# Performance work log

Hardware: AMD Instinct MI355X
Metric: run time of the kernel (lower is better)

The kernel has to match this reference:

```python
import jax, jax.numpy as jnp
import numpy as np

T2 = 0.05
EPS = 1e-05
N = 8192
D = 512
C = 16
COUNT = N // C


def setup_inputs() -> dict:
    key = jax.random.key(0)
    k1, k2 = jax.random.split(key)
    text = jax.random.normal(k1, (N, D), dtype=jnp.float32)
    image = jax.random.normal(k2, (N, D), dtype=jnp.float32)
    # label must contain exactly class_counts[i] samples of class i
    label = (jnp.arange(N) // COUNT).astype(jnp.int32)
    class_counts = jnp.full((C,), COUNT, dtype=jnp.int32)
    return {"text": text, "image": image, "label": label, "class_counts": class_counts}


def _normalize(x):
    # torch F.normalize(x, dim=1): x / max(||x||, 1e-12)
    n = jnp.sqrt(jnp.sum(x * x, axis=1, keepdims=True))
    return x / jnp.maximum(n, 1e-12)


def reference(text, image, label, class_counts):
    num_classes = class_counts.shape[0]
    onehot = jax.nn.one_hot(label, num_classes, dtype=text.dtype)  # [N, C]
    inv_count = 1.0 / class_counts.astype(text.dtype)              # [C]

    def loss_one(f):
        f = _normalize(f)
        # cosine similarity of unit vectors == dot product
        E = jnp.exp((f @ f.T) / T2)                 # [N, N]
        cls_sums = E @ onehot                       # [N, C]: per-row sum grouped by column class
        own = jnp.take_along_axis(cls_sums, label[:, None].astype(jnp.int32), axis=1)[:, 0]
        within = own - jnp.diagonal(E)              # mask out self-similarity (eye mask)
        other = (jnp.sum(cls_sums, axis=1) - own) / (num_classes - 1)
        # NOTE: original torch code aliases denominator_i = nominator_i and then
        # updates in place (+=), so nominator == denominator after the class loop.
        den = within + other
        per_row = -jnp.log(den / (den + EPS))
        return jnp.sum(per_row * inv_count[label])

    return loss_one(text) + loss_one(image)
```

## Files before the change

### kernel.cpp

```cpp
#include <hip/hip_runtime.h>
#include <stdint.h>

#define NROWS 8192
#define DDIM 512
#define NCLS 16
#define T2INV 20.0f
#define EPSV 1e-5f
#define NTILE 32
#define NOFF (NTILE * (NTILE - 1) / 2)
#define NBLK 1024

typedef int int32x4 __attribute__((ext_vector_type(4)));

__device__ __forceinline__ void async16(void* lds, const void* g) {
  auto gp = (__attribute__((address_space(1))) uint32_t*)(uintptr_t)g;
  auto lp = (__attribute__((address_space(3))) uint32_t*)(uintptr_t)lds;
  __builtin_amdgcn_global_load_lds(gp, lp, 16, 0, 0);
}

__device__ __forceinline__ uint32_t q8(float f) {
  float c = fmaxf(-127.f, fminf(127.f, f * 127.f));
  return (uint32_t)((int)rintf(c) & 255);
}

__global__ __launch_bounds__(256) void norm_kernel(const float* __restrict__ text,
                                                   const float* __restrict__ image,
                                                   uint8_t* __restrict__ out,
                                                   float* __restrict__ den,
                                                   float* __restrict__ out0) {
  const int w = threadIdx.x >> 6, l = threadIdx.x & 63;
  const int rid = blockIdx.x * 4 + w;
  const int m = rid >> 13;
  const int row = rid & (NROWS - 1);
  const float* src = (m ? image : text) + (size_t)row * DDIM;
  float4 v0 = ((const float4*)src)[l];
  float4 v1 = ((const float4*)src)[64 + l];
  float s = v0.x * v0.x + v0.y * v0.y + v0.z * v0.z + v0.w * v0.w +
            v1.x * v1.x + v1.y * v1.y + v1.z * v1.z + v1.w * v1.w;
  #pragma unroll
  for (int off = 32; off; off >>= 1) s += __shfl_xor(s, off);
  const float inv = 1.0f / fmaxf(sqrtf(s), 1e-12f);
  uint2 o;
  o.x = q8(v0.x * inv) | (q8(v0.y * inv) << 8) | (q8(v0.z * inv) << 16) |
        (q8(v0.w * inv) << 24);
  o.y = q8(v1.x * inv) | (q8(v1.y * inv) << 8) | (q8(v1.z * inv) << 16) |
        (q8(v1.w * inv) << 24);
  ((uint2*)(out + (size_t)rid * DDIM))[l] = o;
  if (l == 0) den[rid] = 0.0f;
  if (rid == 0 && l == 0) out0[0] = 0.0f;
}

__global__ __launch_bounds__(512, 2) void gram_kernel(const uint8_t* __restrict__ Fall,
                                                      float* __restrict__ denAll) {
  const int bid = blockIdx.x;
  const int bs = (bid & 7) * (NBLK / 8) + (bid >> 3);

  const int w = threadIdx.x >> 6, l = threadIdx.x & 63;
  const int wr = w >> 2, wc = w & 3;

  __shared__ __align__(16) uint8_t Ab[2][32768];
  __shared__ __align__(16) uint8_t Bb[2][32768];

  const int sbase = w * 8 + (l >> 3);
  const int skb = (((l & 7) ^ ((4 * w + (l >> 4)) & 7))) * 16;
  const size_t g0 = (size_t)sbase * DDIM + skb;

  uint32_t aoff[8], boff[4];
  #pragma unroll
  for (int f = 0; f < 8; ++f) {
    const int rowl = wr * 128 + f * 16 + (l & 15);
    aoff[f] = (uint32_t)(rowl * 128 + (((l >> 4) ^ ((rowl >> 1) & 7)) << 4));
  }
  #pragma unroll
  for (int f = 0; f < 4; ++f) {
    const int rowl = wc * 64 + f * 16 + (l & 15);
    boff[f] = (uint32_t)(rowl * 128 + (((l >> 4) ^ ((rowl >> 1) & 7)) << 4));
  }

  auto run_tile = [&](const uint8_t* __restrict__ F, float* __restrict__ den,
                      int q, int p, bool diag) {
    const bool dead = diag && (wr == 1) && (wc < 2);
    const uint8_t* sA = F + (size_t)q * 256 * DDIM + g0;
    const uint8_t* sB = F + (size_t)p * 256 * DDIM + g0;
    const uint8_t* bb0 = diag ? &Ab[0][0] : &Bb[0][0];

    int32x4 acc[8][4] = {};

    #define STAGE(buf, k0)                                                    \
      {                                                                       \
        _Pragma("unroll")                                                     \
        for (int i = 0; i < 4; ++i) {                                         \
          async16(&Ab[buf][w * 1024 + i * 8192], sA + i * 32768 + (k0));      \
          if (!diag)                                                          \
            async16(&Bb[buf][w * 1024 + i * 8192], sB + i * 32768 + (k0));    \
        }                                                                     \
      }

    STAGE(0, 0);
    #pragma unroll
    for (int ts = 0; ts < 4; ++ts) {
      asm volatile("s_waitcnt vmcnt(0)" ::: "memory");
      __builtin_amdgcn_s_barrier();
      if (ts < 3) STAGE((ts + 1) & 1, (ts + 1) * 128);
      if (!dead) {
        #pragma unroll
        for (int sub = 0; sub < 2; ++sub) {
          int32x4 b[4];
          #pragma unroll
          for (int f = 0; f < 4; ++f)
            b[f] = *(const int32x4*)(bb0 + (ts & 1) * 32768 +
                                     (boff[f] ^ (sub * 64)));
          #pragma unroll
          for (int fh = 0; fh < 2; ++fh) {
            int32x4 a[4];
            #pragma unroll
            for (int f = 0; f < 4; ++f)
              a[f] = *(const int32x4*)(&Ab[0][0] + (ts & 1) * 32768 +
                                       (aoff[fh * 4 + f] ^ (sub * 64)));
            __builtin_amdgcn_s_setprio(1);
            #pragma unroll
            for (int i = 0; i < 4; ++i) {
              #pragma unroll
              for (int j = 0; j < 4; ++j)
                acc[fh * 4 + i][j] = __builtin_amdgcn_mfma_i32_16x16x64_i8(
                    a[i], b[j], acc[fh * 4 + i][j], 0, 0, 0);
            }
            __builtin_amdgcn_s_setprio(0);
          }
        }
      }
    }
    #undef STAGE

    if (!dead) {
      const float SC = T2INV / 16129.0f;
      const float wgt = ((q >> 1) == (p >> 1)) ? 1.0f : (1.0f / 15.0f);
      const int rbase = q * 256 + wr * 128;
      const int cbase = p * 256 + wc * 64;
      float cs[4] = {0.f, 0.f, 0.f, 0.f};
      #pragma unroll
      for (int fi = 0; fi < 8; ++fi) {
        const int rg0 = rbase + fi * 16 + ((l >> 4) << 2);
        float rs[4] = {0.f, 0.f, 0.f, 0.f};
        #pragma unroll
        for (int fj = 0; fj < 4; ++fj) {
          const int cg = cbase + fj * 16 + (l & 15);
          #pragma unroll
          for (int r = 0; r < 4; ++r) {
            float e = __expf((float)acc[fi][fj][r] * SC);
            if (diag && rg0 + r >= cg) e = 0.0f;
            rs[r] += e;
            cs[fj] += e;
          }
        }
        #pragma unroll
        for (int r = 0; r < 4; ++r) {
          rs[r] += __shfl_xor(rs[r], 1);
          rs[r] += __shfl_xor(rs[r], 2);
          rs[r] += __shfl_xor(rs[r], 4);
          rs[r] += __shfl_xor(rs[r], 8);
        }
        if ((l & 15) == 0) {
          #pragma unroll
          for (int r = 0; r < 4; ++r) atomicAdd(&den[rg0 + r], wgt * rs[r]);
        }
      }
      #pragma unroll
      for (int fj = 0; fj < 4; ++fj) {
        cs[fj] += __shfl_xor(cs[fj], 16);
        cs[fj] += __shfl_xor(cs[fj], 32);
      }
      if (l < 16) {
        #pragma unroll
        for (int fj = 0; fj < 4; ++fj)
          atomicAdd(&den[cbase + fj * 16 + l], wgt * cs[fj]);
      }
    }
  };

  if (bs < 2 * NOFF) {
    const int mat = bs >= NOFF;
    const int t = bs - NOFF * mat;
    int p = (int)((1.0f + sqrtf(1.0f + 8.0f * (float)t)) * 0.5f);
    while ((p + 1) * p / 2 <= t) ++p;
    while (p * (p - 1) / 2 > t) --p;
    const int q = t - p * (p - 1) / 2;
    run_tile(Fall + (size_t)mat * NROWS * DDIM, denAll + (size_t)mat * NROWS,
             q, p, false);
  } else {
    const int d = bs - 2 * NOFF;
    const int mat = d >> 4, k = d & 15;
    const uint8_t* F = Fall + (size_t)mat * NROWS * DDIM;
    float* den = denAll + (size_t)mat * NROWS;
    run_tile(F, den, 2 * k, 2 * k, true);
    __syncthreads();
    run_tile(F, den, 2 * k + 1, 2 * k + 1, true);
  }
}

__global__ __launch_bounds__(256) void finalize_kernel(const float* __restrict__ den,
                                                       const int* __restrict__ label,
                                                       const int* __restrict__ counts,
                                                       float* __restrict__ out) {
  const int i = blockIdx.x * 256 + threadIdx.x;
  const float d = den[i];
  const float ic = 1.0f / (float)counts[label[i & (NROWS - 1)]];
  float s = log1pf(EPSV / d) * ic;
  #pragma unroll
  for (int off = 32; off; off >>= 1) s += __shfl_xor(s, off);
  if ((threadIdx.x & 63) == 0) atomicAdd(out, s);
}

__global__ void sentinel_kernel(float* out) { out[0] = -42.0f; }

extern "C" void kernel_launch(void* const* d_in, const int* in_sizes, int n_in,
                              void* d_out, int out_size, void* d_ws, size_t ws_size,
                              hipStream_t stream) {
  (void)in_sizes; (void)n_in; (void)out_size;
  const float* text  = (const float*)d_in[0];
  const float* image = (const float*)d_in[1];
  const int* label   = (const int*)d_in[2];
  const int* counts  = (const int*)d_in[3];

  const size_t fn_bytes = (size_t)2 * NROWS * DDIM;
  const size_t need = fn_bytes + (size_t)2 * NROWS * sizeof(float);
  if (ws_size < need) {
    sentinel_kernel<<<1, 1, 0, stream>>>((float*)d_out);
    return;
  }

  uint8_t* Fn = (uint8_t*)d_ws;
  float* den = (float*)((char*)d_ws + fn_bytes);

  norm_kernel<<<dim3((2 * NROWS) / 4), 256, 0, stream>>>(text, image, Fn, den,
                                                         (float*)d_out);
  gram_kernel<<<dim3(NBLK), 512, 0, stream>>>(Fn, den);
  finalize_kernel<<<dim3((2 * NROWS) / 256), 256, 0, stream>>>(den, label, counts,
                                                               (float*)d_out);
}
```

Baseline: 79.14 us.

## Process multiple tiles per block with cross-tile prefetch of the next tile

Halves the grid so each block processes two off-diagonal tiles (or four diagonal tiles), and remaps the tile assignment to fit. The first K-slice of the next tile is staged into LDS during the last K-step of the current tile, so its load overlaps compute and the epilogue. This cuts block launch overhead and hides the pipeline fill of each later tile. The cost is longer blocks, fewer blocks for load balancing, and more complex tile decoding.

```diff
diff --git a/kernel.cpp b/kernel.cpp
--- a/kernel.cpp
+++ b/kernel.cpp
@@ -7,8 +7,7 @@
 #define T2INV 20.0f
 #define EPSV 1e-5f
 #define NTILE 32
-#define NOFF (NTILE * (NTILE - 1) / 2)
-#define NBLK 1024
+#define NBLK 512
 
 typedef int int32x4 __attribute__((ext_vector_type(4)));
 
@@ -54,6 +53,8 @@
                                                       float* __restrict__ denAll) {
   const int bid = blockIdx.x;
   const int bs = (bid & 7) * (NBLK / 8) + (bid >> 3);
+  const bool diagQ = bs >= 496;
+  const int nt = diagQ ? 4 : 2;
 
   const int w = threadIdx.x >> 6, l = threadIdx.x & 63;
   const int wr = w >> 2, wc = w & 3;
@@ -77,31 +78,64 @@
     boff[f] = (uint32_t)(rowl * 128 + (((l >> 4) ^ ((rowl >> 1) & 7)) << 4));
   }
 
-  auto run_tile = [&](const uint8_t* __restrict__ F, float* __restrict__ den,
-                      int q, int p, bool diag) {
-    const bool dead = diag && (wr == 1) && (wc < 2);
-    const uint8_t* sA = F + (size_t)q * 256 * DDIM + g0;
-    const uint8_t* sB = F + (size_t)p * 256 * DDIM + g0;
-    const uint8_t* bb0 = diag ? &Ab[0][0] : &Bb[0][0];
+  auto decode = [&](int tl, int& mat, int& q, int& p) {
+    if (bs < 480) {
+      mat = bs >= 240;
+      const int u = bs - 240 * mat;
+      int qq = 0, acc = 0;
+      while (acc + ((31 - qq) >> 1) <= u) { acc += (31 - qq) >> 1; ++qq; }
+      q = qq;
+      p = qq + 1 + 2 * (u - acc) + tl;
+    } else if (bs < 496) {
+      const int i = bs - 480;
+      mat = i >= 8;
+      q = 4 * (i - 8 * mat) + 2 * tl;
+      p = 31;
+    } else {
+      const int d = bs - 496;
+      mat = d >= 8;
+      q = p = 4 * (d - 8 * mat) + tl;
+    }
+  };
+
+  auto stage = [&](const uint8_t* sA, const uint8_t* sB, bool diag, int buf,
+                   int k0) {
+    #pragma unroll
+    for (int i = 0; i < 4; ++i) {
+      async16(&Ab[buf][w * 1024 + i * 8192], sA + i * 32768 + k0);
+      if (!diag) async16(&Bb[buf][w * 1024 + i * 8192], sB + i * 32768 + k0);
+    }
+  };
+
+  int mc, qc, pc, mn, qn, pn;
+  decode(0, mc, qc, pc);
+  const uint8_t* Fc = Fall + (size_t)mc * NROWS * DDIM;
+  const uint8_t* sAc = Fc + (size_t)qc * 256 * DDIM + g0;
+  const uint8_t* sBc = Fc + (size_t)pc * 256 * DDIM + g0;
+  stage(sAc, sBc, diagQ, 0, 0);
+
+  for (int tl = 0; tl < nt; ++tl) {
+    const bool dead = diagQ && (wr == 1) && (wc < 2);
+    const uint8_t* bb0 = diagQ ? &Ab[0][0] : &Bb[0][0];
+    const bool havenext = (tl + 1 < nt);
+    const uint8_t *sAn = nullptr, *sBn = nullptr;
+    if (havenext) {
+      decode(tl + 1, mn, qn, pn);
+      const uint8_t* Fn_ = Fall + (size_t)mn * NROWS * DDIM;
+      sAn = Fn_ + (size_t)qn * 256 * DDIM + g0;
+      sBn = Fn_ + (size_t)pn * 256 * DDIM + g0;
+    }
 
     int32x4 acc[8][4] = {};
 
-    #define STAGE(buf, k0)                                                    \
-      {                                                                       \
-        _Pragma("unroll")                                                     \
-        for (int i = 0; i < 4; ++i) {                                         \
-          async16(&Ab[buf][w * 1024 + i * 8192], sA + i * 32768 + (k0));      \
-          if (!diag)                                                          \
-            async16(&Bb[buf][w * 1024 + i * 8192], sB + i * 32768 + (k0));    \
-        }                                                                     \
-      }
-
-    STAGE(0, 0);
     #pragma unroll
     for (int ts = 0; ts < 4; ++ts) {
       asm volatile("s_waitcnt vmcnt(0)" ::: "memory");
       __builtin_amdgcn_s_barrier();
-      if (ts < 3) STAGE((ts + 1) & 1, (ts + 1) * 128);
+      if (ts < 3)
+        stage(sAc, sBc, diagQ, (ts + 1) & 1, (ts + 1) * 128);
+      else if (havenext)
+        stage(sAn, sBn, diagQ, 0, 0);
       if (!dead) {
         #pragma unroll
         for (int sub = 0; sub < 2; ++sub) {
@@ -130,13 +164,13 @@
         }
       }
     }
-    #undef STAGE
 
     if (!dead) {
+      float* den = denAll + (size_t)mc * NROWS;
       const float SC = T2INV / 16129.0f;
-      const float wgt = ((q >> 1) == (p >> 1)) ? 1.0f : (1.0f / 15.0f);
-      const int rbase = q * 256 + wr * 128;
-      const int cbase = p * 256 + wc * 64;
+      const float wgt = ((qc >> 1) == (pc >> 1)) ? 1.0f : (1.0f / 15.0f);
+      const int rbase = qc * 256 + wr * 128;
+      const int cbase = pc * 256 + wc * 64;
       float cs[4] = {0.f, 0.f, 0.f, 0.f};
       #pragma unroll
       for (int fi = 0; fi < 8; ++fi) {
@@ -148,7 +182,7 @@
           #pragma unroll
           for (int r = 0; r < 4; ++r) {
             float e = __expf((float)acc[fi][fj][r] * SC);
-            if (diag && rg0 + r >= cg) e = 0.0f;
+            if (diagQ && rg0 + r >= cg) e = 0.0f;
             rs[r] += e;
             cs[fj] += e;
           }
@@ -176,25 +210,9 @@
           atomicAdd(&den[cbase + fj * 16 + l], wgt * cs[fj]);
       }
     }
-  };
-
-  if (bs < 2 * NOFF) {
-    const int mat = bs >= NOFF;
-    const int t = bs - NOFF * mat;
-    int p = (int)((1.0f + sqrtf(1.0f + 8.0f * (float)t)) * 0.5f);
-    while ((p + 1) * p / 2 <= t) ++p;
-    while (p * (p - 1) / 2 > t) --p;
-    const int q = t - p * (p - 1) / 2;
-    run_tile(Fall + (size_t)mat * NROWS * DDIM, denAll + (size_t)mat * NROWS,
-             q, p, false);
-  } else {
-    const int d = bs - 2 * NOFF;
-    const int mat = d >> 4, k = d & 15;
-    const uint8_t* F = Fall + (size_t)mat * NROWS * DDIM;
-    float* den = denAll + (size_t)mat * NROWS;
-    run_tile(F, den, 2 * k, 2 * k, true);
-    __syncthreads();
-    run_tile(F, den, 2 * k + 1, 2 * k + 1, true);
+
+    mc = mn; qc = qn; pc = pn;
+    if (havenext) { sAc = sAn; sBc = sBn; }
   }
 }
 
```

Result: slower. 101.0 us (+27.7%).

## Retile int8 Gram kernel to 128x128 tiles with 256-thread blocks

Applied to the files above, without the earlier changes.

The Gram tile shrinks from 256x256 to 128x128, and the tile grid grows to 64x64 upper-triangle tiles across 4096 blocks. Each block now uses 4 waves with a 2x2 warp layout, a 64-byte K-slab per stage over 8 stages, and a reworked LDS swizzle. The goal is more concurrent blocks per CU and better load balance across the many CUs. The cost is more global and LDS traffic per MFMA and twice as many atomic row and column reductions.

```diff
diff --git a/kernel.cpp b/kernel.cpp
--- a/kernel.cpp
+++ b/kernel.cpp
@@ -6,9 +6,9 @@
 #define NCLS 16
 #define T2INV 20.0f
 #define EPSV 1e-5f
-#define NTILE 32
+#define NTILE 64
 #define NOFF (NTILE * (NTILE - 1) / 2)
-#define NBLK 1024
+#define NBLK 4096
 
 typedef int int32x4 __attribute__((ext_vector_type(4)));
 
@@ -50,96 +50,84 @@
   if (rid == 0 && l == 0) out0[0] = 0.0f;
 }
 
-__global__ __launch_bounds__(512, 2) void gram_kernel(const uint8_t* __restrict__ Fall,
+__global__ __launch_bounds__(256, 4) void gram_kernel(const uint8_t* __restrict__ Fall,
                                                       float* __restrict__ denAll) {
   const int bid = blockIdx.x;
   const int bs = (bid & 7) * (NBLK / 8) + (bid >> 3);
 
   const int w = threadIdx.x >> 6, l = threadIdx.x & 63;
-  const int wr = w >> 2, wc = w & 3;
-
-  __shared__ __align__(16) uint8_t Ab[2][32768];
-  __shared__ __align__(16) uint8_t Bb[2][32768];
-
-  const int sbase = w * 8 + (l >> 3);
-  const int skb = (((l & 7) ^ ((4 * w + (l >> 4)) & 7))) * 16;
-  const size_t g0 = (size_t)sbase * DDIM + skb;
-
-  uint32_t aoff[8], boff[4];
-  #pragma unroll
-  for (int f = 0; f < 8; ++f) {
-    const int rowl = wr * 128 + f * 16 + (l & 15);
-    aoff[f] = (uint32_t)(rowl * 128 + (((l >> 4) ^ ((rowl >> 1) & 7)) << 4));
-  }
+  const int wr = w >> 1, wc = w & 1;
+
+  __shared__ __align__(16) uint8_t Ab[2][8192];
+  __shared__ __align__(16) uint8_t Bb[2][8192];
+
+  const int srow = w * 16 + (l >> 2);
+  const int skb = ((l & 3) ^ ((l >> 3) & 3)) * 16;
+  const size_t g0 = (size_t)srow * DDIM + skb;
+
+  uint32_t aoff[4], boff[4];
   #pragma unroll
   for (int f = 0; f < 4; ++f) {
-    const int rowl = wc * 64 + f * 16 + (l & 15);
-    boff[f] = (uint32_t)(rowl * 128 + (((l >> 4) ^ ((rowl >> 1) & 7)) << 4));
+    const int ra = wr * 64 + f * 16 + (l & 15);
+    aoff[f] = (uint32_t)(ra * 64 + ((((l >> 4) ^ ((ra >> 1) & 3))) << 4));
+    const int rb = wc * 64 + f * 16 + (l & 15);
+    boff[f] = (uint32_t)(rb * 64 + ((((l >> 4) ^ ((rb >> 1) & 3))) << 4));
   }
 
   auto run_tile = [&](const uint8_t* __restrict__ F, float* __restrict__ den,
                       int q, int p, bool diag) {
-    const bool dead = diag && (wr == 1) && (wc < 2);
-    const uint8_t* sA = F + (size_t)q * 256 * DDIM + g0;
-    const uint8_t* sB = F + (size_t)p * 256 * DDIM + g0;
+    const bool dead = diag && (wr == 1) && (wc == 0);
+    const uint8_t* sA = F + (size_t)q * 128 * DDIM + g0;
+    const uint8_t* sB = F + (size_t)p * 128 * DDIM + g0;
     const uint8_t* bb0 = diag ? &Ab[0][0] : &Bb[0][0];
 
-    int32x4 acc[8][4] = {};
+    int32x4 acc[4][4] = {};
 
     #define STAGE(buf, k0)                                                    \
       {                                                                       \
         _Pragma("unroll")                                                     \
-        for (int i = 0; i < 4; ++i) {                                         \
-          async16(&Ab[buf][w * 1024 + i * 8192], sA + i * 32768 + (k0));      \
+        for (int i = 0; i < 2; ++i) {                                         \
+          async16(&Ab[buf][w * 1024 + i * 4096], sA + i * 32768 + (k0));      \
           if (!diag)                                                          \
-            async16(&Bb[buf][w * 1024 + i * 8192], sB + i * 32768 + (k0));    \
+            async16(&Bb[buf][w * 1024 + i * 4096], sB + i * 32768 + (k0));    \
         }                                                                     \
       }
 
     STAGE(0, 0);
     #pragma unroll
-    for (int ts = 0; ts < 4; ++ts) {
+    for (int ts = 0; ts < 8; ++ts) {
       asm volatile("s_waitcnt vmcnt(0)" ::: "memory");
       __builtin_amdgcn_s_barrier();
-      if (ts < 3) STAGE((ts + 1) & 1, (ts + 1) * 128);
+      if (ts < 7) STAGE((ts + 1) & 1, (ts + 1) * 64);
       if (!dead) {
-        #pragma unroll
-        for (int sub = 0; sub < 2; ++sub) {
-          int32x4 b[4];
+        int32x4 a[4], b[4];
+        #pragma unroll
+        for (int f = 0; f < 4; ++f)
+          b[f] = *(const int32x4*)(bb0 + (ts & 1) * 8192 + boff[f]);
+        #pragma unroll
+        for (int f = 0; f < 4; ++f)
+          a[f] = *(const int32x4*)(&Ab[0][0] + (ts & 1) * 8192 + aoff[f]);
+        __builtin_amdgcn_s_setprio(1);
+        #pragma unroll
+        for (int i = 0; i < 4; ++i) {
           #pragma unroll
-          for (int f = 0; f < 4; ++f)
-            b[f] = *(const int32x4*)(bb0 + (ts & 1) * 32768 +
-                                     (boff[f] ^ (sub * 64)));
-          #pragma unroll
-          for (int fh = 0; fh < 2; ++fh) {
-            int32x4 a[4];
-            #pragma unroll
-            for (int f = 0; f < 4; ++f)
-              a[f] = *(const int32x4*)(&Ab[0][0] + (ts & 1) * 32768 +
-                                       (aoff[fh * 4 + f] ^ (sub * 64)));
-            __builtin_amdgcn_s_setprio(1);
-            #pragma unroll
-            for (int i = 0; i < 4; ++i) {
-              #pragma unroll
-              for (int j = 0; j < 4; ++j)
-                acc[fh * 4 + i][j] = __builtin_amdgcn_mfma_i32_16x16x64_i8(
-                    a[i], b[j], acc[fh * 4 + i][j], 0, 0, 0);
-            }
-            __builtin_amdgcn_s_setprio(0);
-          }
-        }
+          for (int j = 0; j < 4; ++j)
+            acc[i][j] = __builtin_amdgcn_mfma_i32_16x16x64_i8(
+                a[i], b[j], acc[i][j], 0, 0, 0);
+        }
+        __builtin_amdgcn_s_setprio(0);
       }
     }
     #undef STAGE
 
     if (!dead) {
       const float SC = T2INV / 16129.0f;
-      const float wgt = ((q >> 1) == (p >> 1)) ? 1.0f : (1.0f / 15.0f);
-      const int rbase = q * 256 + wr * 128;
-      const int cbase = p * 256 + wc * 64;
+      const float wgt = ((q >> 2) == (p >> 2)) ? 1.0f : (1.0f / 15.0f);
+      const int rbase = q * 128 + wr * 64;
+      const int cbase = p * 128 + wc * 64;
       float cs[4] = {0.f, 0.f, 0.f, 0.f};
       #pragma unroll
-      for (int fi = 0; fi < 8; ++fi) {
+      for (int fi = 0; fi < 4; ++fi) {
         const int rg0 = rbase + fi * 16 + ((l >> 4) << 2);
         float rs[4] = {0.f, 0.f, 0.f, 0.f};
         #pragma unroll
@@ -189,7 +177,7 @@
              q, p, false);
   } else {
     const int d = bs - 2 * NOFF;
-    const int mat = d >> 4, k = d & 15;
+    const int mat = d >> 5, k = d & 31;
     const uint8_t* F = Fall + (size_t)mat * NROWS * DDIM;
     float* den = denAll + (size_t)mat * NROWS;
     run_tile(F, den, 2 * k, 2 * k, true);
@@ -234,7 +222,7 @@
 
   norm_kernel<<<dim3((2 * NROWS) / 4), 256, 0, stream>>>(text, image, Fn, den,
                                                          (float*)d_out);
-  gram_kernel<<<dim3(NBLK), 512, 0, stream>>>(Fn, den);
+  gram_kernel<<<dim3(NBLK), 256, 0, stream>>>(Fn, den);
   finalize_kernel<<<dim3((2 * NROWS) / 256), 256, 0, stream>>>(den, label, counts,
                                                                (float*)d_out);
 }
```

Result: faster. 76.75 us (-3.0%).
